# Kernel optimization log

Hardware: AMD Instinct MI355X
Metric: run time of the kernel (lower is better)

The kernel has to match this reference:

```python
import jax, jax.numpy as jnp
import numpy as np
import math

# ----- sizes -----
NUM_EDGES = 16384
NUM_NODES = 1024          # senders index into [0, NUM_NODES)
N_MUL = 64                # multiplicity n = V.shape[1]
AVG_NEIGH = 16.0          # avg_num_neighbors
F_IN = 64                 # scalar feature dim of x

# ----- real spherical harmonics (component normalization: sum_m Y_lm^2 = 2l+1) -----
_S3 = math.sqrt(3.0); _S5 = math.sqrt(5.0); _S15 = math.sqrt(15.0)
_C33 = math.sqrt(70.0)/4.0; _C32 = math.sqrt(105.0)/2.0
_C31 = math.sqrt(42.0)/4.0; _C30 = math.sqrt(7.0)/2.0; _CXYZ = math.sqrt(105.0)

def _sph(vn):
    x, y, z = vn[:, 0], vn[:, 1], vn[:, 2]
    Y0 = jnp.ones_like(x)[:, None]
    Y1 = _S3 * vn
    Y2 = jnp.stack([_S15*x*y, _S15*y*z, 0.5*_S5*(3*z*z - 1), _S15*x*z, 0.5*_S15*(x*x - y*y)], axis=1)
    Y3 = jnp.stack([_C33*y*(3*x*x - y*y), _CXYZ*x*y*z, _C31*y*(5*z*z - 1), _C30*z*(5*z*z - 3), _C31*x*(5*z*z - 1), _C32*z*(x*x - y*y), _C33*x*(x*x - 3*y*y)], axis=1)
    return [Y0, Y1, Y2, Y3]

# monomial form of the same SH, used to derive EXACT Clebsch-Gordan coefficients
_SHP = {
    0: [[(1.0, (0,0,0))]],
    1: [[(_S3, (1,0,0))], [(_S3, (0,1,0))], [(_S3, (0,0,1))]],
    2: [[(_S15, (1,1,0))], [(_S15, (0,1,1))], [(1.5*_S5, (0,0,2)), (-0.5*_S5, (0,0,0))], [(_S15, (1,0,1))], [(0.5*_S15, (2,0,0)), (-0.5*_S15, (0,2,0))]],
    3: [[(3*_C33, (2,1,0)), (-_C33, (0,3,0))], [(_CXYZ, (1,1,1))], [(5*_C31, (0,1,2)), (-_C31, (0,1,0))], [(5*_C30, (0,0,3)), (-3*_C30, (0,0,1))], [(5*_C31, (1,0,2)), (-_C31, (1,0,0))], [(_C32, (2,0,1)), (-_C32, (0,2,1))], [(_C33, (3,0,0)), (-3*_C33, (1,2,0))]],
}

def _dfact(n):
    r = 1
    while n > 1:
        r *= n; n -= 2
    return r

def _mono_int(e):
    # exact integral of x^a y^b z^c over the unit sphere
    a, b, c = e
    if (a % 2) or (b % 2) or (c % 2):
        return 0.0
    return 4.0*math.pi*_dfact(a-1)*_dfact(b-1)*_dfact(c-1)/_dfact(a+b+c+1)

def _pmul(p, q):
    return [(cp*cq, (a1+a2, b1+b2, c1+c2)) for cp, (a1,b1,c1) in p for cq, (a2,b2,c2) in q]

def _pint(p):
    return sum(c*_mono_int(e) for c, e in p)

def _cg(l1, l2, l3):
    # unique SO(3) intertwiner in this real-SH basis, scaled like e3nn component norm: sqrt(2l3+1)*w3j
    C = np.zeros((2*l1+1, 2*l2+1, 2*l3+1))
    for i, p1 in enumerate(_SHP[l1]):
        for j, p2 in enumerate(_SHP[l2]):
            p12 = _pmul(p1, p2)
            for k, p3 in enumerate(_SHP[l3]):
                C[i, j, k] = _pint(_pmul(p12, p3)) / (4.0*math.pi)
    return jnp.asarray(C / np.linalg.norm(C) * np.sqrt(2*l3+1), dtype=jnp.float32)

# tensor-product paths surviving filter_ir_out = 0e + 1o + 2e (inputs: SH 0e+1o+2e+3o, V 0e+1o+2e)
_PATHS0 = [(0,0), (1,1), (2,2)]
_PATHS1 = [(0,1), (1,0), (1,2), (2,1), (3,2)]
_PATHS2 = [(0,2), (1,1), (2,0), (2,2), (3,1)]
CGS = {(l1, l2, l3): _cg(l1, l2, l3) for l3, ps in ((0, _PATHS0), (1, _PATHS1), (2, _PATHS2)) for l1, l2 in ps}

# e3nn normalize_function(silu): divide by sqrt(E_{z~N(0,1)}[silu(z)^2])
_zg = np.linspace(-12.0, 12.0, 200001)
_phi = np.exp(-0.5*_zg*_zg)/np.sqrt(2.0*np.pi)
_sl = _zg/(1.0 + np.exp(-_zg))
ACT_C = float(np.sqrt(np.sum(_sl*_sl*_phi)*(_zg[1]-_zg[0])))

def _nsilu(v):
    return jax.nn.silu(v) / ACT_C

def _forward(vectors, x, V, senders, W_w, W1, W2, W3, Wv1, Wv2):
    E, n = V.shape[0], V.shape[1]
    d = jnp.linalg.norm(vectors, axis=1, keepdims=True)                 # [E,1] edge lengths
    vn = vectors / d
    Y = jnp.concatenate(_sph(vn), axis=1)                               # [E,16], ell = 0..3
    w = (x @ W_w) / math.sqrt(x.shape[1])                               # [E,n] edge weights (1-layer MLP, no act)
    wY = w[:, :, None] * Y[:, None, :]                                  # [E,n,16]
    agg = jax.ops.segment_sum(wY, senders, num_segments=NUM_NODES)[senders]  # scatter_sum + map_back
    agg = agg / math.sqrt(AVG_NEIGH)
    A = jnp.split(agg, [1, 4, 9], axis=2)                               # SH chunks: dims 1,3,5,7
    B = jnp.split(V, [1, 4], axis=2)                                    # V chunks: dims 1,3,5
    def tp(l1, l2, l3):
        return jnp.einsum('eni,enj,ijk->enk', A[l1], B[l2], CGS[(l1, l2, l3)])
    scal = jnp.concatenate([tp(a, b, 0) for a, b in _PATHS0], axis=2)   # [E,n,3] new scalars
    V1 = jnp.concatenate([tp(a, b, 1) for a, b in _PATHS1], axis=1)     # [E,5n,3] 1o paths
    V2 = jnp.concatenate([tp(a, b, 2) for a, b in _PATHS2], axis=1)     # [E,5n,5] 2e paths
    h = jnp.concatenate([x, scal.reshape(E, 3*n)], axis=1)              # [E, F_IN+3n]
    h = _nsilu(h @ W1 / math.sqrt(h.shape[1]))
    h = _nsilu(h @ W2 / math.sqrt(W2.shape[0]))
    h = h @ W3 / math.sqrt(W3.shape[0])                                 # output_activation=False
    # poly_envelope(p-1=5, 2), p=6: 1 - 28 d^6 + 48 d^7 - 21 d^8 on [0,1), 0 outside
    u = 1.0 - 28.0*d**6 + 48.0*d**7 - 21.0*d**8
    x_out = jnp.where(d < 1.0, u, 0.0) * h                              # [E,64]
    o1 = jnp.einsum('emi,mo->eoi', V1, Wv1) / math.sqrt(V1.shape[1])    # Linear per irrep: [E,n,3]
    o2 = jnp.einsum('emi,mo->eoi', V2, Wv2) / math.sqrt(V2.shape[1])    # [E,n,5]
    # output 0e block has no input path -> zeros (e3nn Linear, no bias)
    V_out = jnp.concatenate([jnp.zeros((E, n, 1), x_out.dtype), o1, o2], axis=2)  # [E,n,9]
    return x_out, V_out

def setup_inputs():
    key = jax.random.key(0)
    ks = jax.random.split(key, 10)
    E = NUM_EDGES
    vectors = 0.35 * jax.random.normal(ks[0], (E, 3), jnp.float32)   # mostly inside cutoff radius 1
    x = jax.random.normal(ks[1], (E, F_IN), jnp.float32)
    V = jax.random.normal(ks[2], (E, N_MUL, 9), jnp.float32)
    senders = jax.random.randint(ks[3], (E,), 0, NUM_NODES, dtype=jnp.int32)
    W_w = jax.random.normal(ks[4], (F_IN, N_MUL), jnp.float32)
    W1 = jax.random.normal(ks[5], (F_IN + 3*N_MUL, 64), jnp.float32)
    W2 = jax.random.normal(ks[6], (64, 64), jnp.float32)
    W3 = jax.random.normal(ks[7], (64, 64), jnp.float32)
    Wv1 = jax.random.normal(ks[8], (5*N_MUL, N_MUL), jnp.float32)
    Wv2 = jax.random.normal(ks[9], (5*N_MUL, N_MUL), jnp.float32)
    return {"vectors": vectors, "x": x, "V": V, "senders": senders, "W_w": W_w, "W1": W1, "W2": W2, "W3": W3, "Wv1": Wv1, "Wv2": Wv2}

def reference(vectors, x, V, senders, W_w, W1, W2, W3, Wv1, Wv2):
    return _forward(vectors, x, V, senders, W_w, W1, W2, W3, Wv1, Wv2)
```

## Files before the change

kernel.cpp:

```cpp
#include <hip/hip_runtime.h>
#include <math.h>

#define NNODES 1024
#define EDGES 16384
#define EB 4

typedef __attribute__((ext_vector_type(8))) short short8;
typedef __attribute__((ext_vector_type(4))) float f32x4;

__device__ __forceinline__ unsigned short f2bf(float f) {
  union { float f; unsigned int u; } v; v.f = f;
  unsigned int r = v.u + 0x7fffu + ((v.u >> 16) & 1u);
  return (unsigned short)(r >> 16);
}

__device__ __constant__ int PL1[13] = {0,1,2, 0,1,1,2,3, 0,1,2,2,3};
__device__ __constant__ int PL2[13] = {0,1,2, 1,0,2,1,2, 2,1,0,2,1};
__device__ __constant__ int PL3[13] = {0,0,0, 1,1,1,1,1, 2,2,2,2,2};
__device__ __constant__ int PCG[13] = {0,1,10, 35,44,53,98,143, 248,273,318,343,468};

__device__ __constant__ double SHC[16][2] = {
  {1.0, 0.0},
  {1.7320508075688772, 0.0},
  {1.7320508075688772, 0.0},
  {1.7320508075688772, 0.0},
  {3.8729833462074170, 0.0},
  {3.8729833462074170, 0.0},
  {3.3541019662496844, -1.1180339887498949},
  {3.8729833462074170, 0.0},
  {1.9364916731037085, -1.9364916731037085},
  {6.2749501990055667, -2.0916500663351889},
  {10.246950765959598, 0.0},
  {8.1009258730098255, -1.6201851746019651},
  {6.6143782776614768, -3.9686269665968861},
  {8.1009258730098255, -1.6201851746019651},
  {5.1234753829797990, -5.1234753829797990},
  {2.0916500663351889, -6.2749501990055667},
};
__device__ __constant__ int SHE[16][2] = {
  {0,0},{1,0},{16,0},{256,0},
  {17,0},{272,0},{512,0},{257,0},{2,32},
  {18,48},{273,0},{528,16},{768,256},{513,1},{258,288},{3,33}};

__global__ void k0(int* __restrict__ counts) {
  counts[blockIdx.x*256 + threadIdx.x] = 0;
}

__global__ __launch_bounds__(256) void prep(
    const float* __restrict__ Wv1, const float* __restrict__ Wv2,
    const float* __restrict__ W1, const float* __restrict__ W2, const float* __restrict__ W3,
    unsigned short* __restrict__ wv1f, unsigned short* __restrict__ wv2f,
    unsigned short* __restrict__ w1f, unsigned short* __restrict__ w2f,
    unsigned short* __restrict__ w3f,
    float* __restrict__ cg, float* __restrict__ actp)
{
  const int bid = blockIdx.x;
  const int t = threadIdx.x;

  if (bid < 13) {
    __shared__ double sh[256];
    const int p = bid;
    const int LOFF[4] = {0,1,4,9};
    int l1 = PL1[p], l2 = PL2[p], l3 = PL3[p];
    int n1 = 2*l1+1, n2 = 2*l2+1, n3 = 2*l3+1;
    int nent = n1*n2*n3;
    const unsigned long long DP =
        1ULL | (1ULL<<7) | (1ULL<<14) | (2ULL<<21) | (3ULL<<28)
      | (8ULL<<35) | (15ULL<<42) | (48ULL<<49) | (105ULL<<56);
    double v = 0.0;
    if (t < nent) {
      int i = t / (n2*n3);
      int rem = t - i*(n2*n3);
      int j = rem / n3;
      int k = rem - j*n3;
      int lm1 = LOFF[l1]+i, lm2 = LOFF[l2]+j, lm3 = LOFF[l3]+k;
      double c1a = SHC[lm1][0], c1b = SHC[lm1][1];
      double c2a = SHC[lm2][0], c2b = SHC[lm2][1];
      double c3a = SHC[lm3][0], c3b = SHC[lm3][1];
      int e1a = SHE[lm1][0], e1b = SHE[lm1][1];
      int e2a = SHE[lm2][0], e2b = SHE[lm2][1];
      int e3a = SHE[lm3][0], e3b = SHE[lm3][1];
      double cs1[2] = {c1a, c1b}; int es1[2] = {e1a, e1b};
      double cs2[2] = {c2a, c2b}; int es2[2] = {e2a, e2b};
      double cs3[2] = {c3a, c3b}; int es3[2] = {e3a, e3b};
      #pragma unroll
      for (int t1 = 0; t1 < 2; t1++)
      #pragma unroll
      for (int t2 = 0; t2 < 2; t2++)
      #pragma unroll
      for (int t3 = 0; t3 < 2; t3++) {
        double cc = cs1[t1]*cs2[t2]*cs3[t3];
        int s = es1[t1] + es2[t2] + es3[t3];
        int a = s & 15, b = (s >> 4) & 15, c = (s >> 8) & 15;
        if (!((a|b|c) & 1)) {
          double num = (double)(int)((DP >> (7*a)) & 127)
                     * (double)(int)((DP >> (7*b)) & 127)
                     * (double)(int)((DP >> (7*c)) & 127);
          double den = (double)(int)((DP >> (7*(a+b+c+2))) & 127);
          v += cc * (num / den);
        }
      }
    }
    sh[t] = (t < nent) ? v*v : 0.0;
    __syncthreads();
    for (int d = 128; d > 0; d >>= 1) {
      if (t < d) sh[t] += sh[t+d];
      __syncthreads();
    }
    double scale = sqrt((double)(2*l3+1)) / sqrt(sh[0]);
    if (t < nent) cg[PCG[p] + t] = (float)(v * scale);

  } else if (bid < 21) {
    __shared__ float shf[256];
    const int b = bid - 13;
    const float dz = 24.0f / 200000.0f;
    float s = 0.f;
    for (int i = b*256 + t; i <= 200000; i += 8*256) {
      float z = -12.0f + dz * (float)i;
      float ph = __expf(-0.5f * z * z) * 0.3989422804014327f;
      float sl = z / (1.f + __expf(-z));
      s = fmaf(sl*sl, ph, s);
    }
    shf[t] = s;
    __syncthreads();
    for (int d = 128; d > 0; d >>= 1) {
      if (t < d) shf[t] += shf[t + d];
      __syncthreads();
    }
    if (t == 0) actp[b] = shf[0];

  } else {
    const int wid = t >> 6, lane = t & 63;
    const int g = (bid - 21)*4 + wid;
    const float* src; unsigned short* dst; int nk, f;
    if (g < 40)       { src = Wv1; dst = wv1f; nk = 10; f = g; }
    else if (g < 80)  { src = Wv2; dst = wv2f; nk = 10; f = g - 40; }
    else if (g < 112) { src = W1;  dst = w1f;  nk = 8;  f = g - 80; }
    else if (g < 120) { src = W2;  dst = w2f;  nk = 2;  f = g - 112; }
    else              { src = W3;  dst = w3f;  nk = 2;  f = g - 120; }
    int nt = f / nk;
    int ks = f - nt*nk;
    unsigned short us[8];
    #pragma unroll
    for (int j = 0; j < 8; j++) {
      float v = src[(ks*32 + (lane>>4)*8 + j)*64 + nt*16 + (lane & 15)];
      us[j] = f2bf(v);
    }
    uint4 pk;
    pk.x = (unsigned)us[0] | ((unsigned)us[1] << 16);
    pk.y = (unsigned)us[2] | ((unsigned)us[3] << 16);
    pk.z = (unsigned)us[4] | ((unsigned)us[5] << 16);
    pk.w = (unsigned)us[6] | ((unsigned)us[7] << 16);
    *(uint4*)(dst + ((size_t)f*64 + lane)*8) = pk;
  }
}

__global__ __launch_bounds__(256) void edgepass(
    const float* __restrict__ x, const float* __restrict__ Ww,
    const int* __restrict__ senders,
    float* __restrict__ w_ws, int* __restrict__ counts, int* __restrict__ elist, int E)
{
  const int wid = threadIdx.x >> 6, lane = threadIdx.x & 63;
  const int e = blockIdx.x * 4 + wid;
  if (e >= E) return;
  float xv = x[e*64 + lane];
  float w = 0.f;
  #pragma unroll
  for (int f = 0; f < 64; f++)
    w = fmaf(__shfl(xv, f), Ww[f*64 + lane], w);
  w_ws[e*64 + lane] = w * 0.125f;
  if (lane == 0) {
    int s = senders[e];
    int pos = atomicAdd(&counts[s], 1) & 63;
    elist[s*64 + pos] = e;
  }
}

__global__ __launch_bounds__(256) void k_node(
    const float* __restrict__ vec, const float* __restrict__ w_ws,
    const int* __restrict__ counts, const int* __restrict__ elist,
    float* __restrict__ node_agg)
{
  const int wid = threadIdx.x >> 6, lane = threadIdx.x & 63;
  const int s = blockIdx.x * 4 + wid;
  const int deg = min(counts[s], 64);

  const float S3 = 1.7320508075688772f, S5 = 2.23606797749979f, S15 = 3.872983346207417f;
  const float C33 = 2.091650066335189f, C32 = 5.123475382979799f, C31 = 1.6201851746019651f;
  const float C30 = 1.3228756555322954f, CX = 10.246950765959598f;

  float A[16];
  #pragma unroll
  for (int k = 0; k < 16; k++) A[k] = 0.f;

  for (int ii = 0; ii < deg; ii++) {
    int e = elist[s*64 + ii];
    float vx = vec[e*3+0], vy = vec[e*3+1], vz = vec[e*3+2];
    float d = sqrtf(vx*vx + vy*vy + vz*vz);
    float X = vx/d, Yv = vy/d, Z = vz/d;
    float y[16];
    y[0] = 1.f;
    y[1] = S3*X;  y[2] = S3*Yv;  y[3] = S3*Z;
    y[4] = S15*X*Yv; y[5] = S15*Yv*Z; y[6] = 0.5f*S5*(3.f*Z*Z - 1.f);
    y[7] = S15*X*Z;  y[8] = 0.5f*S15*(X*X - Yv*Yv);
    y[9]  = C33*Yv*(3.f*X*X - Yv*Yv);
    y[10] = CX*X*Yv*Z;
    y[11] = C31*Yv*(5.f*Z*Z - 1.f);
    y[12] = C30*Z*(5.f*Z*Z - 3.f);
    y[13] = C31*X*(5.f*Z*Z - 1.f);
    y[14] = C32*Z*(X*X - Yv*Yv);
    y[15] = C33*X*(X*X - 3.f*Yv*Yv);
    float wv = w_ws[e*64 + lane];
    #pragma unroll
    for (int k = 0; k < 16; k++) A[k] = fmaf(wv, y[k], A[k]);
  }
  float* dst = node_agg + s*1024 + lane*16;
  #pragma unroll
  for (int k = 0; k < 4; k++)
    ((f32x4*)dst)[k] = (f32x4){A[4*k], A[4*k+1], A[4*k+2], A[4*k+3]};
}

template<int L1, int L2, int L3>
__device__ __forceinline__ void tp_path(const float* __restrict__ cgp,
    const float a[16], const float b[9], float o[2*L3+1])
{
  constexpr int N1 = 2*L1+1, N2 = 2*L2+1, N3 = 2*L3+1;
  constexpr int AO = (L1==0) ? 0 : (L1==1) ? 1 : (L1==2) ? 4 : 9;
  constexpr int BO = (L2==0) ? 0 : (L2==1) ? 1 : 4;
  #pragma unroll
  for (int k = 0; k < N3; k++) o[k] = 0.f;
  int ci = 0;
  #pragma unroll
  for (int i = 0; i < N1; i++) {
    #pragma unroll
    for (int j = 0; j < N2; j++) {
      float ab = a[AO+i] * b[BO+j];
      #pragma unroll
      for (int k = 0; k < N3; k++) { o[k] = fmaf(ab, cgp[ci], o[k]); ci++; }
    }
  }
}

__global__ __launch_bounds__(256, 4) void edge_main(
    const float* __restrict__ vec, const float* __restrict__ x,
    const float* __restrict__ V, const int* __restrict__ senders,
    const float* __restrict__ node_agg, const float* __restrict__ cg,
    const unsigned short* __restrict__ wv1f, const unsigned short* __restrict__ wv2f,
    const unsigned short* __restrict__ w1f, const unsigned short* __restrict__ w2f,
    const unsigned short* __restrict__ w3f,
    float* __restrict__ out, int E, const float* __restrict__ actp)
{
  __shared__ __align__(16) unsigned short V1sh[12*328];
  __shared__ __align__(16) unsigned short V2sh[20*328];
  __shared__ __align__(16) unsigned short zrow[336];
  __shared__ __align__(16) unsigned short hsh[4*264];
  __shared__ __align__(16) unsigned short h1sh[4*72];
  __shared__ __align__(16) unsigned short h2sh[4*72];
  __shared__ __align__(16) float vosh[4*584];
  __shared__ float ush[EB];

  const int t = threadIdx.x;
  const int wid = t >> 6, lane = t & 63;
  const int e0 = blockIdx.x * EB;
  const size_t E64 = (size_t)E * 64;
  const float inv_actc = 1.f / sqrtf((actp[0]+actp[1]+actp[2]+actp[3]
                                     +actp[4]+actp[5]+actp[6]+actp[7]) * (24.0f/200000.0f));

  if (t < 168) ((unsigned int*)zrow)[t] = 0u;

  { int el = t >> 6, o = t & 63;
    hsh[el*264 + o] = f2bf(x[(e0+el)*64 + o]); }

  {
    const int eloc = wid;
    const int eg = e0 + eloc;
    const int s = senders[eg];

    float a[16];
    const float* nap = node_agg + s*1024 + lane*16;
    #pragma unroll
    for (int k = 0; k < 16; k++) a[k] = nap[k] * 0.25f;

    float b[9];
    const float* vp = V + (size_t)eg*576 + lane*9;
    #pragma unroll
    for (int j = 0; j < 9; j++) b[j] = vp[j];

    float o1[1], o3[3], o5[5];
    tp_path<0,0,0>(cg + 0,  a, b, o1); hsh[eloc*264 + 64 + lane*3 + 0] = f2bf(o1[0]);
    tp_path<1,1,0>(cg + 1,  a, b, o1); hsh[eloc*264 + 64 + lane*3 + 1] = f2bf(o1[0]);
    tp_path<2,2,0>(cg + 10, a, b, o1); hsh[eloc*264 + 64 + lane*3 + 2] = f2bf(o1[0]);
    tp_path<0,1,1>(cg + 35, a, b, o3);
    { int r = eloc*3; for (int i=0;i<3;i++) V1sh[(r+i)*328 + 0*64 + lane] = f2bf(o3[i]); }
    tp_path<1,0,1>(cg + 44, a, b, o3);
    { int r = eloc*3; for (int i=0;i<3;i++) V1sh[(r+i)*328 + 1*64 + lane] = f2bf(o3[i]); }
    tp_path<1,2,1>(cg + 53, a, b, o3);
    { int r = eloc*3; for (int i=0;i<3;i++) V1sh[(r+i)*328 + 2*64 + lane] = f2bf(o3[i]); }
    tp_path<2,1,1>(cg + 98, a, b, o3);
    { int r = eloc*3; for (int i=0;i<3;i++) V1sh[(r+i)*328 + 3*64 + lane] = f2bf(o3[i]); }
    tp_path<3,2,1>(cg + 143, a, b, o3);
    { int r = eloc*3; for (int i=0;i<3;i++) V1sh[(r+i)*328 + 4*64 + lane] = f2bf(o3[i]); }
    tp_path<0,2,2>(cg + 248, a, b, o5);
    { int r = eloc*5; for (int i=0;i<5;i++) V2sh[(r+i)*328 + 0*64 + lane] = f2bf(o5[i]); }
    tp_path<1,1,2>(cg + 273, a, b, o5);
    { int r = eloc*5; for (int i=0;i<5;i++) V2sh[(r+i)*328 + 1*64 + lane] = f2bf(o5[i]); }
    tp_path<2,0,2>(cg + 318, a, b, o5);
    { int r = eloc*5; for (int i=0;i<5;i++) V2sh[(r+i)*328 + 2*64 + lane] = f2bf(o5[i]); }
    tp_path<2,2,2>(cg + 343, a, b, o5);
    { int r = eloc*5; for (int i=0;i<5;i++) V2sh[(r+i)*328 + 3*64 + lane] = f2bf(o5[i]); }
    tp_path<3,1,2>(cg + 468, a, b, o5);
    { int r = eloc*5; for (int i=0;i<5;i++) V2sh[(r+i)*328 + 4*64 + lane] = f2bf(o5[i]); }

    if (lane == 0) {
      float vx = vec[eg*3+0], vy = vec[eg*3+1], vz = vec[eg*3+2];
      float d = sqrtf(vx*vx + vy*vy + vz*vz);
      float u = 0.f;
      if (d < 1.f) {
        float d3 = d*d*d, d6 = d3*d3, d7 = d6*d, d8 = d7*d;
        u = 1.f - 28.f*d6 + 48.f*d7 - 21.f*d8;
      }
      ush[eloc] = u;
    }
  }
  __syncthreads();

  const int ntile = wid;
  const int qr = lane >> 4;
  const int ml = lane & 15;
  const float s320 = 0.05590169943749474f;

  {
    f32x4 acc = (f32x4){0,0,0,0};
    const unsigned short* p0 = (ml < 12) ? &V1sh[ml*328] : zrow;
    const unsigned short* bb = wv1f + ((size_t)(ntile*10)*64 + lane)*8;
    #pragma unroll
    for (int ks = 0; ks < 10; ks++) {
      short8 bf = *(const short8*)(bb + ks*512);
      short8 af = *(const short8*)(p0 + ks*32 + qr*8);
      acc = __builtin_amdgcn_mfma_f32_16x16x32_bf16(af, bf, acc, 0, 0, 0);
    }
    #pragma unroll
    for (int r = 0; r < 4; r++) {
      int row = qr*4 + r;
      if (row < 12) {
        int el = row / 3, i = row - (row/3)*3;
        vosh[el*584 + (ntile*16+ml)*9 + 1 + i] = acc[r] * s320;
      }
    }
  }

  {
    f32x4 acc[2]; acc[0] = (f32x4){0,0,0,0}; acc[1] = (f32x4){0,0,0,0};
    const unsigned short* p0 = &V2sh[ml*328];
    const unsigned short* p1 = (16+ml < 20) ? &V2sh[(16+ml)*328] : zrow;
    const unsigned short* bb = wv2f + ((size_t)(ntile*10)*64 + lane)*8;
    #pragma unroll
    for (int ks = 0; ks < 10; ks++) {
      short8 bf = *(const short8*)(bb + ks*512);
      int ao = ks*32 + qr*8;
      short8 af0 = *(const short8*)(p0 + ao);
      short8 af1 = *(const short8*)(p1 + ao);
      acc[0] = __builtin_amdgcn_mfma_f32_16x16x32_bf16(af0, bf, acc[0], 0, 0, 0);
      acc[1] = __builtin_amdgcn_mfma_f32_16x16x32_bf16(af1, bf, acc[1], 0, 0, 0);
    }
    #pragma unroll
    for (int mt = 0; mt < 2; mt++) {
      #pragma unroll
      for (int r = 0; r < 4; r++) {
        int row = mt*16 + qr*4 + r;
        if (row < 20) {
          int el = row / 5, i = row - (row/5)*5;
          vosh[el*584 + (ntile*16+ml)*9 + 4 + i] = acc[mt][r] * s320;
        }
      }
    }
  }

  { int el = t >> 6, o = t & 63;
    vosh[el*584 + o*9] = 0.f; }

  const unsigned short* hp = (ml < 4) ? &hsh[ml*264] : zrow;
  {
    f32x4 c = (f32x4){0,0,0,0};
    const unsigned short* bb = w1f + ((size_t)(ntile*8)*64 + lane)*8;
    #pragma unroll
    for (int ks = 0; ks < 8; ks++) {
      short8 bf = *(const short8*)(bb + ks*512);
      short8 af = *(const short8*)(hp + ks*32 + qr*8);
      c = __builtin_amdgcn_mfma_f32_16x16x32_bf16(af, bf, c, 0, 0, 0);
    }
    #pragma unroll
    for (int r = 0; r < 4; r++) {
      int row = qr*4 + r;
      if (row < 4) {
        float v = c[r] * 0.0625f;
        float sv = v / (1.f + expf(-v)) * inv_actc;
        h1sh[row*72 + ntile*16 + ml] = f2bf(sv);
      }
    }
  }
  __syncthreads();
  {
    f32x4 c = (f32x4){0,0,0,0};
    const unsigned short* ap = (ml < 4) ? &h1sh[ml*72] : zrow;
    const unsigned short* bb = w2f + ((size_t)(ntile*2)*64 + lane)*8;
    #pragma unroll
    for (int ks = 0; ks < 2; ks++) {
      short8 bf = *(const short8*)(bb + ks*512);
      short8 af = *(const short8*)(ap + ks*32 + qr*8);
      c = __builtin_amdgcn_mfma_f32_16x16x32_bf16(af, bf, c, 0, 0, 0);
    }
    #pragma unroll
    for (int r = 0; r < 4; r++) {
      int row = qr*4 + r;
      if (row < 4) {
        float v = c[r] * 0.125f;
        float sv = v / (1.f + expf(-v)) * inv_actc;
        h2sh[row*72 + ntile*16 + ml] = f2bf(sv);
      }
    }
  }
  __syncthreads();
  {
    f32x4 c = (f32x4){0,0,0,0};
    const unsigned short* ap = (ml < 4) ? &h2sh[ml*72] : zrow;
    const unsigned short* bb = w3f + ((size_t)(ntile*2)*64 + lane)*8;
    #pragma unroll
    for (int ks = 0; ks < 2; ks++) {
      short8 bf = *(const short8*)(bb + ks*512);
      short8 af = *(const short8*)(ap + ks*32 + qr*8);
      c = __builtin_amdgcn_mfma_f32_16x16x32_bf16(af, bf, c, 0, 0, 0);
    }
    #pragma unroll
    for (int r = 0; r < 4; r++) {
      int row = qr*4 + r;
      if (row < 4) {
        float v = c[r] * 0.125f;
        out[(size_t)(e0+row)*64 + ntile*16 + ml] = ush[row] * v;
      }
    }
  }

  for (int q = t; q < 576; q += 256) {
    int el = q / 144, i4 = q - (q/144)*144;
    ((f32x4*)(out + E64 + (size_t)(e0+el)*576))[i4] = ((f32x4*)(vosh + el*584))[i4];
  }
}

extern "C" void kernel_launch(void* const* d_in, const int* in_sizes, int n_in,
                              void* d_out, int out_size, void* d_ws, size_t ws_size,
                              hipStream_t stream)
{
  const float* vec     = (const float*)d_in[0];
  const float* x       = (const float*)d_in[1];
  const float* V       = (const float*)d_in[2];
  const int*   senders = (const int*)  d_in[3];
  const float* Ww      = (const float*)d_in[4];
  const float* W1      = (const float*)d_in[5];
  const float* W2      = (const float*)d_in[6];
  const float* W3      = (const float*)d_in[7];
  const float* Wv1     = (const float*)d_in[8];
  const float* Wv2     = (const float*)d_in[9];
  float* out = (float*)d_out;
  const int E = in_sizes[0] / 3;

  char* base = (char*)d_ws;
  float* node_agg = (float*)(base);
  float* w_ws     = (float*)(base + (4<<20));
  float* cg       = (float*)(base + (8<<20));
  float* actp     = (float*)(base + (8<<20) + 4096);
  int* counts     = (int*)  (base + (8<<20) + 8192);
  int* elist      = (int*)  (base + (8<<20) + 12288);
  unsigned short* wv1f = (unsigned short*)(base + (8<<20) + 278528);
  unsigned short* wv2f = (unsigned short*)(base + (8<<20) + 319488);
  unsigned short* w1f  = (unsigned short*)(base + (8<<20) + 360448);
  unsigned short* w2f  = (unsigned short*)(base + (8<<20) + 393216);
  unsigned short* w3f  = (unsigned short*)(base + (8<<20) + 401408);

  k0<<<4, 256, 0, stream>>>(counts);
  prep<<<53, 256, 0, stream>>>(Wv1, Wv2, W1, W2, W3,
                               wv1f, wv2f, w1f, w2f, w3f, cg, actp);
  edgepass<<<(E+3)/4, 256, 0, stream>>>(x, Ww, senders, w_ws, counts, elist, E);
  k_node<<<NNODES/4, 256, 0, stream>>>(vec, w_ws, counts, elist, node_agg);
  edge_main<<<E/EB, 256, 0, stream>>>(vec, x, V, senders, node_agg, cg,
                                      wv1f, wv2f, w1f, w2f, w3f, out, E, actp);
}
```

Baseline: 188.0 us.

## Fold counts reset into prep, split node aggregation across waves, skip zero CG terms

Zeroing of the per-node counts moves into the prep kernel, which removes one kernel launch. k_node now uses one block per node: its four waves each take a strided share of the node's edges, and the partial sums are reduced through shared memory. This aims to cut the serial per-wave edge loop and improve parallelism, at the cost of a __syncthreads and 16KB of LDS per block. The tensor-product path also uses a compile-time parity table to skip FMAs whose Clebsch-Gordan coefficients are structurally zero.

```diff
diff --git a/kernel.cpp b/kernel.cpp
--- a/kernel.cpp
+++ b/kernel.cpp
@@ -42,22 +42,19 @@
   {17,0},{272,0},{512,0},{257,0},{2,32},
   {18,48},{273,0},{528,16},{768,256},{513,1},{258,288},{3,33}};
 
-__global__ void k0(int* __restrict__ counts) {
-  counts[blockIdx.x*256 + threadIdx.x] = 0;
-}
-
 __global__ __launch_bounds__(256) void prep(
     const float* __restrict__ Wv1, const float* __restrict__ Wv2,
     const float* __restrict__ W1, const float* __restrict__ W2, const float* __restrict__ W3,
     unsigned short* __restrict__ wv1f, unsigned short* __restrict__ wv2f,
     unsigned short* __restrict__ w1f, unsigned short* __restrict__ w2f,
     unsigned short* __restrict__ w3f,
-    float* __restrict__ cg, float* __restrict__ actp)
+    float* __restrict__ cg, float* __restrict__ actp, int* __restrict__ counts)
 {
   const int bid = blockIdx.x;
   const int t = threadIdx.x;
 
   if (bid < 13) {
+    if (bid < 4) counts[bid*256 + t] = 0;
     __shared__ double sh[256];
     const int p = bid;
     const int LOFF[4] = {0,1,4,9};
@@ -74,15 +71,9 @@
       int j = rem / n3;
       int k = rem - j*n3;
       int lm1 = LOFF[l1]+i, lm2 = LOFF[l2]+j, lm3 = LOFF[l3]+k;
-      double c1a = SHC[lm1][0], c1b = SHC[lm1][1];
-      double c2a = SHC[lm2][0], c2b = SHC[lm2][1];
-      double c3a = SHC[lm3][0], c3b = SHC[lm3][1];
-      int e1a = SHE[lm1][0], e1b = SHE[lm1][1];
-      int e2a = SHE[lm2][0], e2b = SHE[lm2][1];
-      int e3a = SHE[lm3][0], e3b = SHE[lm3][1];
-      double cs1[2] = {c1a, c1b}; int es1[2] = {e1a, e1b};
-      double cs2[2] = {c2a, c2b}; int es2[2] = {e2a, e2b};
-      double cs3[2] = {c3a, c3b}; int es3[2] = {e3a, e3b};
+      double cs1[2] = {SHC[lm1][0], SHC[lm1][1]}; int es1[2] = {SHE[lm1][0], SHE[lm1][1]};
+      double cs2[2] = {SHC[lm2][0], SHC[lm2][1]}; int es2[2] = {SHE[lm2][0], SHE[lm2][1]};
+      double cs3[2] = {SHC[lm3][0], SHC[lm3][1]}; int es3[2] = {SHE[lm3][0], SHE[lm3][1]};
       #pragma unroll
       for (int t1 = 0; t1 < 2; t1++)
       #pragma unroll
@@ -181,8 +172,9 @@
     const int* __restrict__ counts, const int* __restrict__ elist,
     float* __restrict__ node_agg)
 {
+  __shared__ float red[4*1024];
   const int wid = threadIdx.x >> 6, lane = threadIdx.x & 63;
-  const int s = blockIdx.x * 4 + wid;
+  const int s = blockIdx.x;
   const int deg = min(counts[s], 64);
 
   const float S3 = 1.7320508075688772f, S5 = 2.23606797749979f, S15 = 3.872983346207417f;
@@ -193,7 +185,7 @@
   #pragma unroll
   for (int k = 0; k < 16; k++) A[k] = 0.f;
 
-  for (int ii = 0; ii < deg; ii++) {
+  for (int ii = wid; ii < deg; ii += 4) {
     int e = elist[s*64 + ii];
     float vx = vec[e*3+0], vy = vec[e*3+1], vz = vec[e*3+2];
     float d = sqrtf(vx*vx + vy*vy + vz*vz);
@@ -214,10 +206,16 @@
     #pragma unroll
     for (int k = 0; k < 16; k++) A[k] = fmaf(wv, y[k], A[k]);
   }
-  float* dst = node_agg + s*1024 + lane*16;
   #pragma unroll
-  for (int k = 0; k < 4; k++)
-    ((f32x4*)dst)[k] = (f32x4){A[4*k], A[4*k+1], A[4*k+2], A[4*k+3]};
+  for (int k = 0; k < 16; k++) red[wid*1024 + lane*16 + k] = A[k];
+  __syncthreads();
+  const int t = threadIdx.x;
+  f32x4 v0 = ((f32x4*)red)[t];
+  f32x4 v1 = ((f32x4*)red)[256 + t];
+  f32x4 v2 = ((f32x4*)red)[512 + t];
+  f32x4 v3 = ((f32x4*)red)[768 + t];
+  f32x4 sum = v0 + v1 + v2 + v3;
+  ((f32x4*)(node_agg + (size_t)s*1024))[t] = sum;
 }
 
 template<int L1, int L2, int L3>
@@ -227,6 +225,11 @@
   constexpr int N1 = 2*L1+1, N2 = 2*L2+1, N3 = 2*L3+1;
   constexpr int AO = (L1==0) ? 0 : (L1==1) ? 1 : (L1==2) ? 4 : 9;
   constexpr int BO = (L2==0) ? 0 : (L2==1) ? 1 : 4;
+  constexpr int LM1 = (L1==0) ? 0 : (L1==1) ? 1 : (L1==2) ? 4 : 9;
+  constexpr int LM2 = (L2==0) ? 0 : (L2==1) ? 1 : 4;
+  constexpr int LM3 = (L3==0) ? 0 : (L3==1) ? 1 : 4;
+  static constexpr unsigned char PAR[16] =
+      {0, 1,2,4, 3,6,0,5,0, 2,7,2,4,1,4,1};
   #pragma unroll
   for (int k = 0; k < N3; k++) o[k] = 0.f;
   int ci = 0;
@@ -236,7 +239,11 @@
     for (int j = 0; j < N2; j++) {
       float ab = a[AO+i] * b[BO+j];
       #pragma unroll
-      for (int k = 0; k < N3; k++) { o[k] = fmaf(ab, cgp[ci], o[k]); ci++; }
+      for (int k = 0; k < N3; k++) {
+        if ((PAR[LM1+i] ^ PAR[LM2+j] ^ PAR[LM3+k]) == 0)
+          o[k] = fmaf(ab, cgp[ci], o[k]);
+        ci++;
+      }
     }
   }
 }
@@ -477,11 +484,10 @@
   unsigned short* w2f  = (unsigned short*)(base + (8<<20) + 393216);
   unsigned short* w3f  = (unsigned short*)(base + (8<<20) + 401408);
 
-  k0<<<4, 256, 0, stream>>>(counts);
   prep<<<53, 256, 0, stream>>>(Wv1, Wv2, W1, W2, W3,
-                               wv1f, wv2f, w1f, w2f, w3f, cg, actp);
+                               wv1f, wv2f, w1f, w2f, w3f, cg, actp, counts);
   edgepass<<<(E+3)/4, 256, 0, stream>>>(x, Ww, senders, w_ws, counts, elist, E);
-  k_node<<<NNODES/4, 256, 0, stream>>>(vec, w_ws, counts, elist, node_agg);
+  k_node<<<NNODES, 256, 0, stream>>>(vec, w_ws, counts, elist, node_agg);
   edge_main<<<E/EB, 256, 0, stream>>>(vec, x, V, senders, node_agg, cg,
                                       wv1f, wv2f, w1f, w2f, w3f, out, E, actp);
 }
```

Result: faster. 169.2 us (-10.0%).
